# Kernel optimization log

Measured on AMD Instinct MI355X. Metric: run time of the kernel, lower is better.

Reference implementation:

```python
import jax, jax.numpy as jnp
import numpy as np

B, S, D_IN, D_OUT = 4, 2048, 4096, 4096


def setup_inputs() -> dict:
    key = jax.random.key(0)
    k_x, k_w, k_s, k_b = jax.random.split(key, 4)
    x = jax.random.normal(k_x, (B, S, D_IN), dtype=jnp.float32)
    # ternary weights in {-1, 0, +1}, stored as int (int8 in torch)
    weight_quant = jax.random.randint(k_w, (D_OUT, D_IN), 0, 3, dtype=jnp.int32) - 1
    weight_scale = jax.random.normal(k_s, (D_OUT, 1), dtype=jnp.float32)
    bias = jax.random.normal(k_b, (D_OUT,), dtype=jnp.float32)
    return {"x": x, "weight_quant": weight_quant, "weight_scale": weight_scale, "bias": bias}


def reference(x, weight_quant, weight_scale, bias):
    # dequantize: per-output-row scale applied to ternary weights -> [out, in]
    weight_fp = weight_quant.astype(x.dtype) * weight_scale
    # x @ W^T + b : [B, S, in] x [out, in] -> [B, S, out]
    return jnp.einsum('bsi,oi->bso', x, weight_fp) + bias
```

## Files before the change

kernel.cpp:

```cpp
#include <hip/hip_runtime.h>


#define MDIM 8192
#define NDIM 4096
#define KDIM 4096
#define BM 128
#define BN 128
#define BK 64

typedef __bf16 bf16x8 __attribute__((ext_vector_type(8)));
typedef float f32x4 __attribute__((ext_vector_type(4)));

__device__ __forceinline__ unsigned f2bf_pack(float lo, float hi) {
    unsigned a = __float_as_uint(lo);
    unsigned b = __float_as_uint(hi);
    a += 0x7FFFu + ((a >> 16) & 1u);
    b += 0x7FFFu + ((b >> 16) & 1u);
    return (a >> 16) | (b & 0xFFFF0000u);
}

__device__ __forceinline__ unsigned w2bf_pack(int lo, int hi) {
    unsigned a = __float_as_uint((float)lo) >> 16;
    unsigned b = __float_as_uint((float)hi) & 0xFFFF0000u;
    return a | b;
}

__device__ __forceinline__ void async_load16(const void* gptr, void* lptr) {
    __builtin_amdgcn_global_load_lds(
        (const __attribute__((address_space(1))) void*)gptr,
        (__attribute__((address_space(3))) void*)lptr, 16, 0, 0);
}

#define XGROUPS ((MDIM * (size_t)KDIM) / 8)
#define WGROUPS ((NDIM * (size_t)KDIM) / 8)

__global__ void convert_all(const float* __restrict__ X, const int* __restrict__ Wq,
                            uint4* __restrict__ Xb, uint4* __restrict__ Wb) {
    const size_t gid = (size_t)blockIdx.x * blockDim.x + threadIdx.x;
    if (gid < XGROUPS) {
        const f32x4 a = ((const f32x4*)X)[2 * gid];
        const f32x4 b = ((const f32x4*)X)[2 * gid + 1];
        Xb[gid] = make_uint4(f2bf_pack(a.x, a.y), f2bf_pack(a.z, a.w),
                             f2bf_pack(b.x, b.y), f2bf_pack(b.z, b.w));
    } else {
        const size_t wi = gid - XGROUPS;
        const int4 a = ((const int4*)Wq)[2 * wi];
        const int4 b = ((const int4*)Wq)[2 * wi + 1];
        Wb[wi] = make_uint4(w2bf_pack(a.x, a.y), w2bf_pack(a.z, a.w),
                            w2bf_pack(b.x, b.y), w2bf_pack(b.z, b.w));
    }
}


__global__ __launch_bounds__(256)
void gemm_bf16(const unsigned short* __restrict__ Xb,
               const unsigned short* __restrict__ Wb,
               const float* __restrict__ scale,
               const float* __restrict__ bias,
               float* __restrict__ Out) {
    __shared__ unsigned short As[2][BM * BK];
    __shared__ unsigned short Bs[2][BN * BK];

    const int tid  = threadIdx.x;
    const int lane = tid & 63;
    const int wave = tid >> 6;
    const int quad = lane >> 4;
    const int l16  = lane & 15;
    const int wm   = (wave >> 1) * 64;
    const int wn   = (wave & 1) * 64;

    const int m0 = blockIdx.y * BM;
    const int n0 = blockIdx.x * BN;

    const int lr = lane >> 3;
    const int lc = lane & 7;
    const int cc = lc ^ lr;

    const unsigned short* pA[4];
    const unsigned short* pB[4];
    char* ldsA[2][4];
    char* ldsB[2][4];
#pragma unroll
    for (int j = 0; j < 4; j++) {
        const int rlocal = wave * 32 + j * 8 + lr;
        pA[j] = Xb + (size_t)(m0 + rlocal) * KDIM + cc * 8;
        pB[j] = Wb + (size_t)(n0 + rlocal) * KDIM + cc * 8;
#pragma unroll
        for (int b = 0; b < 2; b++) {
            ldsA[b][j] = (char*)As[b] + (wave * 32 + j * 8) * 128;
            ldsB[b][j] = (char*)Bs[b] + (wave * 32 + j * 8) * 128;
        }
    }

    f32x4 acc[4][4];
#pragma unroll
    for (int i = 0; i < 4; i++)
#pragma unroll
        for (int j = 0; j < 4; j++)
            acc[i][j] = (f32x4){0.f, 0.f, 0.f, 0.f};

    const int sw = l16 & 7;

    auto prefetch = [&](int kt, int buf) {
#pragma unroll
        for (int j = 0; j < 4; j++) async_load16(pA[j] + kt, ldsA[buf][j]);
#pragma unroll
        for (int j = 0; j < 4; j++) async_load16(pB[j] + kt, ldsB[buf][j]);
    };

    auto compute = [&](int buf) {
#pragma unroll
        for (int h = 0; h < 2; h++) {
            bf16x8 af[4], bf[4];
#pragma unroll
            for (int mt = 0; mt < 4; mt++) {
                const int row = wm + mt * 16 + l16;
                af[mt] = *(const bf16x8*)((const char*)As[buf] + row * 128 +
                                          ((h * 4 + quad) ^ sw) * 16);
            }
#pragma unroll
            for (int nt = 0; nt < 4; nt++) {
                const int row = wn + nt * 16 + l16;
                bf[nt] = *(const bf16x8*)((const char*)Bs[buf] + row * 128 +
                                          ((h * 4 + quad) ^ sw) * 16);
            }
#pragma unroll
            for (int mt = 0; mt < 4; mt++)
#pragma unroll
                for (int nt = 0; nt < 4; nt++)
                    acc[mt][nt] = __builtin_amdgcn_mfma_f32_16x16x32_bf16(
                        af[mt], bf[nt], acc[mt][nt], 0, 0, 0);
        }
    };

    prefetch(0, 0);
    __syncthreads();

    for (int kt = 0; kt < KDIM; kt += 2 * BK) {
        prefetch(kt + BK, 1);
        compute(0);
        __syncthreads();
        if (kt + 2 * BK < KDIM) prefetch(kt + 2 * BK, 0);
        compute(1);
        __syncthreads();
    }

#pragma unroll
    for (int nt = 0; nt < 4; nt++) {
        const int n = n0 + wn + nt * 16 + l16;
        const float sc = scale[n];
        const float bi = bias[n];
#pragma unroll
        for (int mt = 0; mt < 4; mt++) {
#pragma unroll
            for (int r = 0; r < 4; r++) {
                const int m = m0 + wm + mt * 16 + quad * 4 + r;
                Out[(size_t)m * NDIM + n] = acc[mt][nt][r] * sc + bi;
            }
        }
    }
}


#define LDSS 72

__global__ __launch_bounds__(256, 2)
void ternary_gemm_fused(const float* __restrict__ X, const int* __restrict__ Wq,
                        const float* __restrict__ scale, const float* __restrict__ bias,
                        float* __restrict__ Out) {
    __shared__ unsigned short As[BM * LDSS];
    __shared__ unsigned short Bs[BN * LDSS];

    const int tid  = threadIdx.x;
    const int lane = tid & 63;
    const int wave = tid >> 6;
    const int quad = lane >> 4;
    const int l16  = lane & 15;
    const int wm   = (wave >> 1) * 64;
    const int wn   = (wave & 1) * 64;

    const int m0 = blockIdx.y * BM;
    const int n0 = blockIdx.x * BN;

    const int srow = tid >> 4;
    const int scol = (tid & 15) * 4;

    const float* Aptr = X  + (size_t)(m0 + srow) * KDIM + scol;
    const int*   Bptr = Wq + (size_t)(n0 + srow) * KDIM + scol;

    f32x4 acc[4][4];
#pragma unroll
    for (int i = 0; i < 4; i++)
#pragma unroll
        for (int j = 0; j < 4; j++)
            acc[i][j] = (f32x4){0.f, 0.f, 0.f, 0.f};

    for (int kt = 0; kt < KDIM; kt += BK) {
        uint2 apk[8], bpk[8];
#pragma unroll
        for (int j = 0; j < 8; j++) {
            const f32x4 av = *(const f32x4*)(Aptr + (size_t)j * 16 * KDIM + kt);
            apk[j].x = f2bf_pack(av.x, av.y);
            apk[j].y = f2bf_pack(av.z, av.w);
        }
#pragma unroll
        for (int j = 0; j < 8; j++) {
            const int4 bv = *(const int4*)(Bptr + (size_t)j * 16 * KDIM + kt);
            bpk[j].x = w2bf_pack(bv.x, bv.y);
            bpk[j].y = w2bf_pack(bv.z, bv.w);
        }
        __syncthreads();
#pragma unroll
        for (int j = 0; j < 8; j++) {
            *(uint2*)&As[(srow + j * 16) * LDSS + scol] = apk[j];
            *(uint2*)&Bs[(srow + j * 16) * LDSS + scol] = bpk[j];
        }
        __syncthreads();

#pragma unroll
        for (int h = 0; h < 2; h++) {
            bf16x8 af[4], bf[4];
#pragma unroll
            for (int mt = 0; mt < 4; mt++)
                af[mt] = *(const bf16x8*)&As[(wm + mt * 16 + l16) * LDSS + h * 32 + quad * 8];
#pragma unroll
            for (int nt = 0; nt < 4; nt++)
                bf[nt] = *(const bf16x8*)&Bs[(wn + nt * 16 + l16) * LDSS + h * 32 + quad * 8];
#pragma unroll
            for (int mt = 0; mt < 4; mt++)
#pragma unroll
                for (int nt = 0; nt < 4; nt++)
                    acc[mt][nt] = __builtin_amdgcn_mfma_f32_16x16x32_bf16(
                        af[mt], bf[nt], acc[mt][nt], 0, 0, 0);
        }
    }

#pragma unroll
    for (int nt = 0; nt < 4; nt++) {
        const int n = n0 + wn + nt * 16 + l16;
        const float sc = scale[n];
        const float bi = bias[n];
#pragma unroll
        for (int mt = 0; mt < 4; mt++) {
#pragma unroll
            for (int r = 0; r < 4; r++) {
                const int m = m0 + wm + mt * 16 + quad * 4 + r;
                Out[(size_t)m * NDIM + n] = acc[mt][nt][r] * sc + bi;
            }
        }
    }
}

extern "C" void kernel_launch(void* const* d_in, const int* in_sizes, int n_in,
                              void* d_out, int out_size, void* d_ws, size_t ws_size,
                              hipStream_t stream) {
    const float* x     = (const float*)d_in[0];
    const int*   wq    = (const int*)d_in[1];
    const float* scale = (const float*)d_in[2];
    const float* bias  = (const float*)d_in[3];
    float* out = (float*)d_out;

    const size_t xb_bytes = (size_t)MDIM * KDIM * 2;
    const size_t wb_bytes = (size_t)NDIM * KDIM * 2;

    if (ws_size >= xb_bytes + wb_bytes) {
        unsigned short* Xb = (unsigned short*)d_ws;
        unsigned short* Wb = (unsigned short*)((char*)d_ws + xb_bytes);

        const size_t total_groups = XGROUPS + WGROUPS;
        convert_all<<<(unsigned)(total_groups / 256), 256, 0, stream>>>(
            x, wq, (uint4*)Xb, (uint4*)Wb);

        dim3 grid(NDIM / BN, MDIM / BM);
        gemm_bf16<<<grid, dim3(256), 0, stream>>>(Xb, Wb, scale, bias, out);
    } else {
        dim3 grid(NDIM / BN, MDIM / BM);
        ternary_gemm_fused<<<grid, dim3(256), 0, stream>>>(x, wq, scale, bias, out);
    }
}
```

Baseline: 583.1 us.

## Replace bf16 GEMM with 256x256-tile, 8-wave, phase-interleaved pipelined kernel

```diff
diff --git a/kernel.cpp b/kernel.cpp
--- a/kernel.cpp
+++ b/kernel.cpp
@@ -4,12 +4,12 @@
 #define MDIM 8192
 #define NDIM 4096
 #define KDIM 4096
-#define BM 128
-#define BN 128
-#define BK 64
+#define NT   64
 
 typedef __bf16 bf16x8 __attribute__((ext_vector_type(8)));
 typedef float f32x4 __attribute__((ext_vector_type(4)));
+
+#define BAR() asm volatile("s_barrier" ::: "memory")
 
 __device__ __forceinline__ unsigned f2bf_pack(float lo, float hi) {
     unsigned a = __float_as_uint(lo);
@@ -52,116 +52,197 @@
 }
 
 
-__global__ __launch_bounds__(256)
-void gemm_bf16(const unsigned short* __restrict__ Xb,
-               const unsigned short* __restrict__ Wb,
-               const float* __restrict__ scale,
-               const float* __restrict__ bias,
-               float* __restrict__ Out) {
-    __shared__ unsigned short As[2][BM * BK];
-    __shared__ unsigned short Bs[2][BN * BK];
+#define RDA(b_, P_, mt_, kh_) (*(const bf16x8*)((const char*)As + (b_)*32768 + \
+        (P_)*4096 + (mt_)*2048 + ((kh_) ? aB1 : aB0)))
+#define RDB(b_, nt_, kh_)     (*(const bf16x8*)((const char*)Bs + (b_)*32768 + \
+        (nt_)*2048 + ((kh_) ? bB1 : bB0)))
+
+__global__ __launch_bounds__(512)
+void gemm_bf16_8ph(const unsigned short* __restrict__ Xb,
+                   const unsigned short* __restrict__ Wb,
+                   const float* __restrict__ scale,
+                   const float* __restrict__ bias,
+                   float* __restrict__ Out) {
+    __shared__ unsigned short As[2 * 2 * 128 * 64];
+    __shared__ unsigned short Bs[2 * 2 * 128 * 64];
 
     const int tid  = threadIdx.x;
     const int lane = tid & 63;
     const int wave = tid >> 6;
+    const int wm   = wave >> 2;
+    const int wn   = wave & 3;
     const int quad = lane >> 4;
     const int l16  = lane & 15;
-    const int wm   = (wave >> 1) * 64;
-    const int wn   = (wave & 1) * 64;
-
-    const int m0 = blockIdx.y * BM;
-    const int n0 = blockIdx.x * BN;
-
-    const int lr = lane >> 3;
-    const int lc = lane & 7;
-    const int cc = lc ^ lr;
-
-    const unsigned short* pA[4];
-    const unsigned short* pB[4];
-    char* ldsA[2][4];
-    char* ldsB[2][4];
-#pragma unroll
-    for (int j = 0; j < 4; j++) {
-        const int rlocal = wave * 32 + j * 8 + lr;
-        pA[j] = Xb + (size_t)(m0 + rlocal) * KDIM + cc * 8;
-        pB[j] = Wb + (size_t)(n0 + rlocal) * KDIM + cc * 8;
-#pragma unroll
-        for (int b = 0; b < 2; b++) {
-            ldsA[b][j] = (char*)As[b] + (wave * 32 + j * 8) * 128;
-            ldsB[b][j] = (char*)Bs[b] + (wave * 32 + j * 8) * 128;
-        }
-    }
-
-    f32x4 acc[4][4];
-#pragma unroll
-    for (int i = 0; i < 4; i++)
-#pragma unroll
-        for (int j = 0; j < 4; j++)
+    const int lr   = lane >> 3;
+    const int cc   = (lane & 7) ^ lr;
+
+    int lid = blockIdx.y * 16 + blockIdx.x;
+    lid = (lid & 7) * 64 + (lid >> 3);
+    const int n0 = (lid & 15) << 8;
+    const int m0 = (lid >> 4) << 8;
+
+    const unsigned short* pA[2][2];
+    const unsigned short* pB[2][2];
+#pragma unroll
+    for (int h = 0; h < 2; ++h)
+#pragma unroll
+        for (int j = 0; j < 2; ++j) {
+            pA[h][j] = Xb + (size_t)(m0 + h * 128 + j * 64 + wave * 8 + lr) * KDIM + cc * 8;
+            pB[h][j] = Wb + (size_t)(n0 + h * 128 + j * 64 + wave * 8 + lr) * KDIM + cc * 8;
+        }
+
+    f32x4 acc[8][4];
+#pragma unroll
+    for (int i = 0; i < 8; ++i)
+#pragma unroll
+        for (int j = 0; j < 4; ++j)
             acc[i][j] = (f32x4){0.f, 0.f, 0.f, 0.f};
 
-    const int sw = l16 & 7;
-
-    auto prefetch = [&](int kt, int buf) {
-#pragma unroll
-        for (int j = 0; j < 4; j++) async_load16(pA[j] + kt, ldsA[buf][j]);
-#pragma unroll
-        for (int j = 0; j < 4; j++) async_load16(pB[j] + kt, ldsB[buf][j]);
+    const int aoff = l16 * 128 + ((quad ^ (l16 & 7)) << 4);
+    const int aB0  = (wm << 14) + aoff;
+    const int aB1  = aB0 ^ 64;
+    const int bB0  = ((wn >> 1) << 14) + ((wn & 1) << 13) + aoff;
+    const int bB1  = bB0 ^ 64;
+
+    auto stageA = [&](int t, int h, int b) {
+        char* d = (char*)As + ((b * 2 + h) << 14) + wave * 1024;
+        async_load16(pA[h][0] + (size_t)t * 64, d);
+        async_load16(pA[h][1] + (size_t)t * 64, d + 8192);
     };
-
-    auto compute = [&](int buf) {
-#pragma unroll
-        for (int h = 0; h < 2; h++) {
-            bf16x8 af[4], bf[4];
-#pragma unroll
-            for (int mt = 0; mt < 4; mt++) {
-                const int row = wm + mt * 16 + l16;
-                af[mt] = *(const bf16x8*)((const char*)As[buf] + row * 128 +
-                                          ((h * 4 + quad) ^ sw) * 16);
-            }
-#pragma unroll
-            for (int nt = 0; nt < 4; nt++) {
-                const int row = wn + nt * 16 + l16;
-                bf[nt] = *(const bf16x8*)((const char*)Bs[buf] + row * 128 +
-                                          ((h * 4 + quad) ^ sw) * 16);
-            }
-#pragma unroll
-            for (int mt = 0; mt < 4; mt++)
-#pragma unroll
-                for (int nt = 0; nt < 4; nt++)
-                    acc[mt][nt] = __builtin_amdgcn_mfma_f32_16x16x32_bf16(
-                        af[mt], bf[nt], acc[mt][nt], 0, 0, 0);
-        }
+    auto stageB = [&](int t, int h, int b) {
+        char* d = (char*)Bs + ((b * 2 + h) << 14) + wave * 1024;
+        async_load16(pB[h][0] + (size_t)t * 64, d);
+        async_load16(pB[h][1] + (size_t)t * 64, d + 8192);
     };
 
-    prefetch(0, 0);
-    __syncthreads();
-
-    for (int kt = 0; kt < KDIM; kt += 2 * BK) {
-        prefetch(kt + BK, 1);
-        compute(0);
-        __syncthreads();
-        if (kt + 2 * BK < KDIM) prefetch(kt + 2 * BK, 0);
-        compute(1);
-        __syncthreads();
-    }
-
-#pragma unroll
-    for (int nt = 0; nt < 4; nt++) {
-        const int n = n0 + wn + nt * 16 + l16;
+    auto tile = [&](int t, int b) {
+        bf16x8 bfr[4][2];
+        {
+            bf16x8 af[2][2];
+#pragma unroll
+            for (int mt = 0; mt < 2; ++mt) {
+                af[mt][0] = RDA(b, 0, mt, 0);
+                af[mt][1] = RDA(b, 0, mt, 1);
+            }
+#pragma unroll
+            for (int nt = 0; nt < 4; ++nt) {
+                bfr[nt][0] = RDB(b, nt, 0);
+                bfr[nt][1] = RDB(b, nt, 1);
+            }
+            if (t + 1 < NT) stageA(t + 1, 0, b ^ 1);
+            BAR();
+            __builtin_amdgcn_s_setprio(1);
+#pragma unroll
+            for (int kh = 0; kh < 2; ++kh)
+#pragma unroll
+                for (int mt = 0; mt < 2; ++mt)
+#pragma unroll
+                    for (int nt = 0; nt < 4; ++nt)
+                        acc[mt][nt] = __builtin_amdgcn_mfma_f32_16x16x32_bf16(
+                            af[mt][kh], bfr[nt][kh], acc[mt][nt], 0, 0, 0);
+            __builtin_amdgcn_s_setprio(0);
+            BAR();
+        }
+        {
+            bf16x8 af[2][2];
+#pragma unroll
+            for (int mt = 0; mt < 2; ++mt) {
+                af[mt][0] = RDA(b, 1, mt, 0);
+                af[mt][1] = RDA(b, 1, mt, 1);
+            }
+            if (t + 1 < NT) stageA(t + 1, 1, b ^ 1);
+            BAR();
+            __builtin_amdgcn_s_setprio(1);
+#pragma unroll
+            for (int kh = 0; kh < 2; ++kh)
+#pragma unroll
+                for (int mt = 0; mt < 2; ++mt)
+#pragma unroll
+                    for (int nt = 0; nt < 4; ++nt)
+                        acc[2 + mt][nt] = __builtin_amdgcn_mfma_f32_16x16x32_bf16(
+                            af[mt][kh], bfr[nt][kh], acc[2 + mt][nt], 0, 0, 0);
+            __builtin_amdgcn_s_setprio(0);
+            BAR();
+        }
+        {
+            bf16x8 af[2][2];
+#pragma unroll
+            for (int mt = 0; mt < 2; ++mt) {
+                af[mt][0] = RDA(b, 2, mt, 0);
+                af[mt][1] = RDA(b, 2, mt, 1);
+            }
+            if (t + 2 < NT) stageB(t + 2, 0, b);
+            BAR();
+            __builtin_amdgcn_s_setprio(1);
+#pragma unroll
+            for (int kh = 0; kh < 2; ++kh)
+#pragma unroll
+                for (int mt = 0; mt < 2; ++mt)
+#pragma unroll
+                    for (int nt = 0; nt < 4; ++nt)
+                        acc[4 + mt][nt] = __builtin_amdgcn_mfma_f32_16x16x32_bf16(
+                            af[mt][kh], bfr[nt][kh], acc[4 + mt][nt], 0, 0, 0);
+            __builtin_amdgcn_s_setprio(0);
+            BAR();
+        }
+        {
+            bf16x8 af[2][2];
+#pragma unroll
+            for (int mt = 0; mt < 2; ++mt) {
+                af[mt][0] = RDA(b, 3, mt, 0);
+                af[mt][1] = RDA(b, 3, mt, 1);
+            }
+            if (t + 2 < NT) stageB(t + 2, 1, b);
+            if (t < NT - 2) asm volatile("s_waitcnt vmcnt(4)" ::: "memory");
+            else            asm volatile("s_waitcnt vmcnt(0)" ::: "memory");
+            BAR();
+            __builtin_amdgcn_s_setprio(1);
+#pragma unroll
+            for (int kh = 0; kh < 2; ++kh)
+#pragma unroll
+                for (int mt = 0; mt < 2; ++mt)
+#pragma unroll
+                    for (int nt = 0; nt < 4; ++nt)
+                        acc[6 + mt][nt] = __builtin_amdgcn_mfma_f32_16x16x32_bf16(
+                            af[mt][kh], bfr[nt][kh], acc[6 + mt][nt], 0, 0, 0);
+            __builtin_amdgcn_s_setprio(0);
+            BAR();
+        }
+    };
+
+    stageA(0, 0, 0); stageA(0, 1, 0); stageB(0, 0, 0); stageB(0, 1, 0);
+    stageB(1, 0, 1); stageB(1, 1, 1);
+    asm volatile("s_waitcnt vmcnt(4)" ::: "memory");
+    BAR();
+
+    for (int tt = 0; tt < NT; tt += 2) {
+        tile(tt, 0);
+        tile(tt + 1, 1);
+    }
+
+#pragma unroll
+    for (int nt = 0; nt < 4; ++nt) {
+        const int n = n0 + wn * 64 + nt * 16 + l16;
         const float sc = scale[n];
         const float bi = bias[n];
 #pragma unroll
-        for (int mt = 0; mt < 4; mt++) {
-#pragma unroll
-            for (int r = 0; r < 4; r++) {
-                const int m = m0 + wm + mt * 16 + quad * 4 + r;
-                Out[(size_t)m * NDIM + n] = acc[mt][nt][r] * sc + bi;
-            }
-        }
-    }
-}
-
-
+        for (int mf = 0; mf < 8; ++mf) {
+#pragma unroll
+            for (int r = 0; r < 4; ++r) {
+                const int m = m0 + wm * 128 + mf * 16 + quad * 4 + r;
+                Out[(size_t)m * NDIM + n] = acc[mf][nt][r] * sc + bi;
+            }
+        }
+    }
+}
+
+#undef RDA
+#undef RDB
+
+
+#define BM 128
+#define BN 128
+#define BK 64
 #define LDSS 72
 
 __global__ __launch_bounds__(256, 2)
@@ -271,8 +352,8 @@
         convert_all<<<(unsigned)(total_groups / 256), 256, 0, stream>>>(
             x, wq, (uint4*)Xb, (uint4*)Wb);
 
-        dim3 grid(NDIM / BN, MDIM / BM);
-        gemm_bf16<<<grid, dim3(256), 0, stream>>>(Xb, Wb, scale, bias, out);
+        dim3 grid(NDIM / 256, MDIM / 256);
+        gemm_bf16_8ph<<<grid, dim3(512), 0, stream>>>(Xb, Wb, scale, bias, out);
     } else {
         dim3 grid(NDIM / BN, MDIM / BM);
         ternary_gemm_fused<<<grid, dim3(256), 0, stream>>>(x, wq, scale, bias, out);
```

Result: faster. 513.6 us (-11.9%).
